# Kernel optimization log

Hardware: AMD Instinct MI355X
Metric: run time of the kernel (lower is better)

Reference implementation:

```python
import jax, jax.numpy as jnp
import numpy as np

EMBED_DIM = 1024
NUM_HEADS = 16
HEAD_DIM = EMBED_DIM // NUM_HEADS
ROPE_BASE = 10000.0


def _rope_cos_sin(seq_len, dim, dtype=jnp.float32):
    inv_freq = 1.0 / (ROPE_BASE ** (jnp.arange(0, dim, 2, dtype=jnp.float32) / dim))
    pos = jnp.arange(seq_len, dtype=jnp.float32)
    freqs = jnp.outer(pos, inv_freq)              # [S, dim/2]
    emb = jnp.concatenate([freqs, freqs], axis=-1)  # [S, dim]
    return jnp.cos(emb).astype(dtype), jnp.sin(emb).astype(dtype)


def _rotate_half(x):
    half = x.shape[-1] // 2
    return jnp.concatenate([-x[..., half:], x[..., :half]], axis=-1)


def setup_inputs() -> dict:
    key = jax.random.key(0)
    ks = jax.random.split(key, 12)
    B, S, E = 4, 2048, EMBED_DIM
    std = 1.0 / np.sqrt(E)
    inp = {
        'query': jax.random.normal(ks[0], (B, S, E), jnp.float32),
        'key': jax.random.normal(ks[1], (B, S, E), jnp.float32),
        'value': jax.random.normal(ks[2], (B, S, E), jnp.float32),
        'Wq': jax.random.uniform(ks[3], (E, E), jnp.float32, -std, std),
        'bq': jax.random.uniform(ks[4], (E,), jnp.float32, -std, std),
        'Wk': jax.random.uniform(ks[5], (E, E), jnp.float32, -std, std),
        'bk': jax.random.uniform(ks[6], (E,), jnp.float32, -std, std),
        'Wv': jax.random.uniform(ks[7], (E, E), jnp.float32, -std, std),
        'bv': jax.random.uniform(ks[8], (E,), jnp.float32, -std, std),
        'Wo': jax.random.uniform(ks[9], (E, E), jnp.float32, -std, std),
        'bo': jax.random.uniform(ks[10], (E,), jnp.float32, -std, std),
    }
    return inp


def reference(query, key, value, Wq, bq, Wk, bk, Wv, bv, Wo, bo):
    B, Sq, E = query.shape
    Sk = key.shape[1]
    H, D = NUM_HEADS, HEAD_DIM
    scale = D ** -0.5

    q = query @ Wq.T + bq
    k = key @ Wk.T + bk
    v = value @ Wv.T + bv

    # [B, H, S, D]
    q = q.reshape(B, Sq, H, D).transpose(0, 2, 1, 3)
    k = k.reshape(B, Sk, H, D).transpose(0, 2, 1, 3)
    v = v.reshape(B, Sk, H, D).transpose(0, 2, 1, 3)

    cos, sin = _rope_cos_sin(Sq, D, q.dtype)  # [S, D]; module slices by seq_len_q for both
    cos = cos[None, None]  # [1,1,S,D]
    sin = sin[None, None]
    q = q * cos + _rotate_half(q) * sin
    k = k * cos + _rotate_half(k) * sin

    scores = jnp.einsum('bhqd,bhkd->bhqk', q, k) * scale
    attn = jax.nn.softmax(scores, axis=-1)  # dropout p=0.0 -> identity
    out = jnp.einsum('bhqk,bhkd->bhqd', attn, v)
    out = out.transpose(0, 2, 1, 3).reshape(B, Sq, E)
    out = out @ Wo.T + bo
    attn_avg = attn.mean(axis=1)  # [B, Sq, Sk]
    return out, attn_avg
```

## Files before the change

kernel.cpp:

```cpp
#include <hip/hip_runtime.h>
#include <math.h>

#define TB 4
#define TS 2048
#define TE 1024
#define TH 16
#define TD 64
#define TM_ (TB*TS)

#define WS_Q   0
#define WS_K   8388608
#define WS_L   16777216
#define WS_TAB 16908288

typedef __attribute__((ext_vector_type(8))) short bf16x8;
typedef __attribute__((ext_vector_type(4))) float f32x4;

static __device__ inline unsigned fbits(float x) {
    union { float f; unsigned u; } v; v.f = x; return v.u;
}
static __device__ inline float bits2f(unsigned u) {
    union { unsigned u; float f; } v; v.u = u; return v.f;
}
static __device__ inline unsigned pack_rhu(float a, float b) {
    return __builtin_amdgcn_perm(fbits(b) + 0x8000u, fbits(a) + 0x8000u, 0x07060302u);
}
static __device__ inline short bf16s(float x) {
    return (short)((fbits(x) + 0x8000u) >> 16);
}
static __device__ inline void split2(float x0, float x1, unsigned& hp, unsigned& lp) {
    unsigned u0 = fbits(x0) + 0x8000u, u1 = fbits(x1) + 0x8000u;
    hp = __builtin_amdgcn_perm(u1, u0, 0x07060302u);
    float h0 = bits2f(u0 & 0xffff0000u);
    float h1 = bits2f(u1 & 0xffff0000u);
    lp = pack_rhu(x0 - h0, x1 - h1);
}

__global__ __launch_bounds__(256, 4)
void wsplit(const float* __restrict__ W0, const float* __restrict__ W1,
            const float* __restrict__ W2, const float* __restrict__ W3,
            short* __restrict__ dst)
{
    const int idx = blockIdx.x * 256 + threadIdx.x;
    const int t = idx & 31;
    const int n = (idx >> 5) & 1023;
    const int w = idx >> 15;
    const float* W = (w == 0) ? W0 : (w == 1) ? W1 : (w == 2) ? W2 : W3;
    const float* sp = W + (size_t)n * 1024 + t * 32;
    short* dp = dst + ((size_t)(w * 1024 + n)) * 2048 + t * 64;
    #pragma unroll
    for (int c = 0; c < 4; ++c) {
        float4 a = *(const float4*)(sp + c * 8);
        float4 b = *(const float4*)(sp + c * 8 + 4);
        unsigned H[4], L[4];
        split2(a.x, a.y, H[0], L[0]);
        split2(a.z, a.w, H[1], L[1]);
        split2(b.x, b.y, H[2], L[2]);
        split2(b.z, b.w, H[3], L[3]);
        *(uint4*)(dp + c * 8)      = make_uint4(H[0], H[1], H[2], H[3]);
        *(uint4*)(dp + 32 + c * 8) = make_uint4(L[0], L[1], L[2], L[3]);
    }
}

template<int MODE>
__global__ __launch_bounds__(256, 2)
void gemm_nt(const float* __restrict__ X, const short* __restrict__ Wsp,
             const float* __restrict__ bias, float* __restrict__ out)
{
    __shared__ short Ah[128][40], Al[128][40];
    __shared__ short Bh[128][40], Bl[128][40];

    const int tid  = threadIdx.x;
    const int lane = tid & 63;
    const int wv   = tid >> 6;
    const int t16  = lane & 15;
    const int quad = lane >> 4;
    const int wm   = (wv >> 1) * 64;
    const int wn   = (wv & 1) * 64;
    const int m0 = blockIdx.y * 128;
    const int n0 = blockIdx.x * 128;
    const int K = TE, N = TE;

    const int srow = tid >> 1;
    const int skc  = (tid & 1) * 16;
    const float* Xp = X + (size_t)(m0 + srow) * K + skc;
    const short* Wp = Wsp + (size_t)(n0 + srow) * 2048 + skc;

    f32x4 acc[4][4];
    #pragma unroll
    for (int i = 0; i < 4; ++i)
        #pragma unroll
        for (int j = 0; j < 4; ++j) acc[i][j] = (f32x4){0.f, 0.f, 0.f, 0.f};

    for (int kt = 0; kt < K; kt += 32) {
        __syncthreads();
        {
            const float* xp = Xp + kt;
            float4 x0 = *(const float4*)(xp);
            float4 x1 = *(const float4*)(xp + 4);
            float4 x2 = *(const float4*)(xp + 8);
            float4 x3 = *(const float4*)(xp + 12);
            const short* wp = Wp + kt * 2;
            uint4 wh0 = *(const uint4*)(wp);
            uint4 wh1 = *(const uint4*)(wp + 8);
            uint4 wl0 = *(const uint4*)(wp + 32);
            uint4 wl1 = *(const uint4*)(wp + 40);

            unsigned H[8], L[8];
            split2(x0.x, x0.y, H[0], L[0]);
            split2(x0.z, x0.w, H[1], L[1]);
            split2(x1.x, x1.y, H[2], L[2]);
            split2(x1.z, x1.w, H[3], L[3]);
            split2(x2.x, x2.y, H[4], L[4]);
            split2(x2.z, x2.w, H[5], L[5]);
            split2(x3.x, x3.y, H[6], L[6]);
            split2(x3.z, x3.w, H[7], L[7]);
            *(uint4*)&Ah[srow][skc]     = make_uint4(H[0], H[1], H[2], H[3]);
            *(uint4*)&Ah[srow][skc + 8] = make_uint4(H[4], H[5], H[6], H[7]);
            *(uint4*)&Al[srow][skc]     = make_uint4(L[0], L[1], L[2], L[3]);
            *(uint4*)&Al[srow][skc + 8] = make_uint4(L[4], L[5], L[6], L[7]);

            *(uint4*)&Bh[srow][skc]     = wh0;
            *(uint4*)&Bh[srow][skc + 8] = wh1;
            *(uint4*)&Bl[srow][skc]     = wl0;
            *(uint4*)&Bl[srow][skc + 8] = wl1;
        }
        __syncthreads();

        bf16x8 ah[4], al[4], bh[4], bl[4];
        #pragma unroll
        for (int i = 0; i < 4; ++i) {
            ah[i] = *(const bf16x8*)&Ah[wm + i * 16 + t16][quad * 8];
            al[i] = *(const bf16x8*)&Al[wm + i * 16 + t16][quad * 8];
            bh[i] = *(const bf16x8*)&Bh[wn + i * 16 + t16][quad * 8];
            bl[i] = *(const bf16x8*)&Bl[wn + i * 16 + t16][quad * 8];
        }
        #pragma unroll
        for (int i = 0; i < 4; ++i)
            #pragma unroll
            for (int j = 0; j < 4; ++j) {
                acc[i][j] = __builtin_amdgcn_mfma_f32_16x16x32_bf16(ah[i], bh[j], acc[i][j], 0, 0, 0);
                acc[i][j] = __builtin_amdgcn_mfma_f32_16x16x32_bf16(al[i], bh[j], acc[i][j], 0, 0, 0);
                acc[i][j] = __builtin_amdgcn_mfma_f32_16x16x32_bf16(ah[i], bl[j], acc[i][j], 0, 0, 0);
            }
    }

    if (MODE == 2) {
        short* o16 = (short*)out;
        const int b = m0 >> 11;
        const int sbase0 = (m0 & 2047) + wm + quad * 4;
        #pragma unroll
        for (int j = 0; j < 4; ++j) {
            const int n = n0 + wn + j * 16 + t16;
            const int h = n >> 6, d = n & 63;
            const float bv = bias[n];
            const size_t base = ((size_t)(b * TH + h) * TD + d) * TS;
            #pragma unroll
            for (int i = 0; i < 4; ++i) {
                const int s = sbase0 + i * 16;
                uint2 p = make_uint2(pack_rhu(acc[i][j][0] + bv, acc[i][j][1] + bv),
                                     pack_rhu(acc[i][j][2] + bv, acc[i][j][3] + bv));
                *(uint2*)(o16 + base + s) = p;
            }
        }
        return;
    }

    #pragma unroll
    for (int j = 0; j < 4; ++j) {
        const int n = n0 + wn + j * 16 + t16;
        const float bv = bias[n];
        if (MODE == 0) {
            #pragma unroll
            for (int i = 0; i < 4; ++i)
                #pragma unroll
                for (int r = 0; r < 4; ++r) {
                    const int m = m0 + wm + i * 16 + quad * 4 + r;
                    out[(size_t)m * N + n] = acc[i][j][r] + bv;
                }
        } else {
            const int h = n >> 6, d = n & 63;
            #pragma unroll
            for (int i = 0; i < 4; ++i)
                #pragma unroll
                for (int r = 0; r < 4; ++r) {
                    const int m = m0 + wm + i * 16 + quad * 4 + r;
                    const int bb_ = m >> 11, s = m & 2047;
                    out[((size_t)(bb_ * TH + h) * TS + s) * TD + d] = acc[i][j][r] + bv;
                }
        }
    }
}

__global__ void rope_table(float* __restrict__ tab)
{
    const int idx = blockIdx.x * 256 + threadIdx.x;
    const int d = idx & 31, s = idx >> 5;
    const float e = (float)(2 * d) / 64.0f;
    const float inv = 1.0f / powf(10000.0f, e);
    const float a = (float)s * inv;
    tab[2 * idx + 0] = cosf(a);
    tab[2 * idx + 1] = sinf(a);
}

__global__ __launch_bounds__(256, 2)
void rope_split(float* __restrict__ Q, float* __restrict__ Kv,
                const float* __restrict__ tab)
{
    const int idx = blockIdx.x * 256 + threadIdx.x;
    const int s  = idx & 2047;
    const int bh = (idx >> 11) & 63;
    const int qk = idx >> 17;
    float* P = qk ? Kv : Q;
    const float scale = qk ? 1.0f : (0.125f * 1.44269504f);
    const int key = qk ? (s & 7) : 0;
    unsigned* rp = (unsigned*)(P + ((size_t)bh * TS + s) * 64);

    unsigned xu[64];
    #pragma unroll
    for (int i = 0; i < 16; ++i) {
        uint4 v = *(const uint4*)(rp + i * 4);
        xu[4 * i + 0] = v.x; xu[4 * i + 1] = v.y;
        xu[4 * i + 2] = v.z; xu[4 * i + 3] = v.w;
    }
    const float* tb = tab + (size_t)s * 64;
    #pragma unroll
    for (int d = 0; d < 32; ++d) {
        const float c = tb[2 * d], sn = tb[2 * d + 1];
        const float x0 = bits2f(xu[d]), x1 = bits2f(xu[d + 32]);
        xu[d]      = fbits((x0 * c - x1 * sn) * scale);
        xu[d + 32] = fbits((x1 * c + x0 * sn) * scale);
    }
    #pragma unroll
    for (int ch = 0; ch < 8; ++ch) {
        unsigned h[4], l[4];
        #pragma unroll
        for (int p = 0; p < 4; ++p)
            split2(bits2f(xu[ch * 8 + 2 * p]), bits2f(xu[ch * 8 + 2 * p + 1]), h[p], l[p]);
        const int slot = ch ^ key;
        *(uint4*)(rp + slot * 4)      = make_uint4(h[0], h[1], h[2], h[3]);
        *(uint4*)(rp + 32 + slot * 4) = make_uint4(l[0], l[1], l[2], l[3]);
    }
}

__global__ __launch_bounds__(512, 4)
void attn_flash(const short* __restrict__ Qs, const short* __restrict__ Ks,
                const short* __restrict__ VT, float* __restrict__ O,
                float* __restrict__ Ls)
{
    __shared__ short KhL[4096], KlL[4096];
    __shared__ short VtL[4096];
    __shared__ short PsL[8192];

    const int tid  = threadIdx.x;
    const int lane = tid & 63;
    const int wv   = tid >> 6;
    const int t16  = lane & 15;
    const int quad = lane >> 4;
    const int q0w  = wv * 16;

    const int L   = blockIdx.x + 16 * blockIdx.y + 256 * blockIdx.z;
    const int xcd = L & 7;
    const int i_  = L >> 3;
    const int qt  = i_ & 15;
    const int g   = (xcd << 3) | (i_ >> 4);
    const int h   = g & 15;
    const int b   = g >> 4;

    const int q0 = qt * 128;
    const int bh = b * TH + h;
    const short* Krb = Ks + (size_t)bh * TS * 128;
    const short* Vth = VT + (size_t)bh * TD * TS;

    const int cx0 = ((quad) ^ (t16 & 7)) * 8;
    const int cx1 = ((4 + quad) ^ (t16 & 7)) * 8;

    bf16x8 qfh[2], qfl[2];
    {
        const short* qrow = Qs + ((size_t)bh * TS + q0 + q0w + t16) * 128;
        qfh[0] = *(const bf16x8*)(qrow + quad * 8);
        qfh[1] = *(const bf16x8*)(qrow + 32 + quad * 8);
        qfl[0] = *(const bf16x8*)(qrow + 64 + quad * 8);
        qfl[1] = *(const bf16x8*)(qrow + 96 + quad * 8);
    }

    float lsum[4] = {0.f, 0.f, 0.f, 0.f};
    f32x4 o_acc[4];
    #pragma unroll
    for (int dt = 0; dt < 4; ++dt) o_acc[dt] = (f32x4){0.f, 0.f, 0.f, 0.f};

    const int krow = tid >> 3;
    const int kch  = tid & 7;
    const int ksl  = (kch ^ (krow & 7)) * 8;

    uint4 rkh = *(const uint4*)(Krb + (size_t)krow * 128 + kch * 8);
    uint4 rkl = *(const uint4*)(Krb + (size_t)krow * 128 + 64 + kch * 8);
    uint4 rvv = *(const uint4*)(Vth + (size_t)krow * TS + kch * 8);

    for (int j0 = 0; j0 < TS; j0 += 64) {
        __syncthreads();
        *(uint4*)&KhL[krow * 64 + kch * 8] = rkh;
        *(uint4*)&KlL[krow * 64 + kch * 8] = rkl;
        *(uint4*)&VtL[krow * 64 + ksl]     = rvv;
        __syncthreads();

        if (j0 + 64 < TS) {
            const short* kr = Krb + (size_t)(j0 + 64 + krow) * 128;
            rkh = *(const uint4*)(kr + kch * 8);
            rkl = *(const uint4*)(kr + 64 + kch * 8);
            rvv = *(const uint4*)(Vth + (size_t)krow * TS + j0 + 64 + kch * 8);
        }

        f32x4 sc[4];
        #pragma unroll
        for (int t = 0; t < 4; ++t) sc[t] = (f32x4){0.f, 0.f, 0.f, 0.f};
        #pragma unroll
        for (int t = 0; t < 4; ++t) {
            const int rb = (t * 16 + t16) * 64;
            bf16x8 kh0 = *(const bf16x8*)&KhL[rb + cx0];
            bf16x8 kl0 = *(const bf16x8*)&KlL[rb + cx0];
            sc[t] = __builtin_amdgcn_mfma_f32_16x16x32_bf16(qfh[0], kh0, sc[t], 0, 0, 0);
            sc[t] = __builtin_amdgcn_mfma_f32_16x16x32_bf16(qfh[0], kl0, sc[t], 0, 0, 0);
            sc[t] = __builtin_amdgcn_mfma_f32_16x16x32_bf16(qfl[0], kh0, sc[t], 0, 0, 0);
            bf16x8 kh1 = *(const bf16x8*)&KhL[rb + cx1];
            bf16x8 kl1 = *(const bf16x8*)&KlL[rb + cx1];
            sc[t] = __builtin_amdgcn_mfma_f32_16x16x32_bf16(qfh[1], kh1, sc[t], 0, 0, 0);
            sc[t] = __builtin_amdgcn_mfma_f32_16x16x32_bf16(qfh[1], kl1, sc[t], 0, 0, 0);
            sc[t] = __builtin_amdgcn_mfma_f32_16x16x32_bf16(qfl[1], kh1, sc[t], 0, 0, 0);
        }

        #pragma unroll
        for (int t = 0; t < 4; ++t) {
            float p0 = __builtin_amdgcn_exp2f(sc[t][0]);
            float p1 = __builtin_amdgcn_exp2f(sc[t][1]);
            float p2 = __builtin_amdgcn_exp2f(sc[t][2]);
            float p3 = __builtin_amdgcn_exp2f(sc[t][3]);
            lsum[0] += p0; lsum[1] += p1; lsum[2] += p2; lsum[3] += p3;
            const int cb = 2 * t + (t16 >> 3);
            const int co = t16 & 7;
            const int r0 = q0w + quad * 4;
            PsL[(r0 + 0) * 64 + ((cb ^ ((r0 + 0) & 7)) * 8) + co] = bf16s(p0);
            PsL[(r0 + 1) * 64 + ((cb ^ ((r0 + 1) & 7)) * 8) + co] = bf16s(p1);
            PsL[(r0 + 2) * 64 + ((cb ^ ((r0 + 2) & 7)) * 8) + co] = bf16s(p2);
            PsL[(r0 + 3) * 64 + ((cb ^ ((r0 + 3) & 7)) * 8) + co] = bf16s(p3);
        }

        {
            const int pr = (q0w + t16) * 64;
            bf16x8 pa0 = *(const bf16x8*)&PsL[pr + cx0];
            #pragma unroll
            for (int dt = 0; dt < 4; ++dt) {
                bf16x8 vb = *(const bf16x8*)&VtL[(dt * 16 + t16) * 64 + cx0];
                o_acc[dt] = __builtin_amdgcn_mfma_f32_16x16x32_bf16(pa0, vb, o_acc[dt], 0, 0, 0);
            }
            bf16x8 pa1 = *(const bf16x8*)&PsL[pr + cx1];
            #pragma unroll
            for (int dt = 0; dt < 4; ++dt) {
                bf16x8 vb = *(const bf16x8*)&VtL[(dt * 16 + t16) * 64 + cx1];
                o_acc[dt] = __builtin_amdgcn_mfma_f32_16x16x32_bf16(pa1, vb, o_acc[dt], 0, 0, 0);
            }
        }
    }

    #pragma unroll
    for (int r = 0; r < 4; ++r) {
        #pragma unroll
        for (int off = 1; off < 16; off <<= 1)
            lsum[r] += __shfl_xor(lsum[r], off, 16);
    }

    #pragma unroll
    for (int r = 0; r < 4; ++r) {
        const int row = q0 + q0w + quad * 4 + r;
        const float inv = 1.0f / lsum[r];
        #pragma unroll
        for (int dt = 0; dt < 4; ++dt)
            O[((size_t)(b * TS) + row) * TE + h * TD + dt * 16 + t16] = o_acc[dt][r] * inv;
        if (t16 == 0)
            Ls[(size_t)bh * TS + row] = lsum[r];
    }
}

__global__ __launch_bounds__(256, 2)
void attn_avg_k(const short* __restrict__ Qs, const short* __restrict__ Ks,
                const float* __restrict__ Ls, float* __restrict__ AV)
{
    __shared__ short Qt[128][72];
    __shared__ short Kt[128][72];
    __shared__ float ML[TH][128];

    const int tid  = threadIdx.x;
    const int lane = tid & 63;
    const int wv   = tid >> 6;
    const int t16  = lane & 15;
    const int quad = lane >> 4;
    const int wq = (wv >> 1) * 64;
    const int wj = (wv & 1) * 64;

    const int j0 = blockIdx.x * 128;
    const int q0 = blockIdx.y * 128;
    const int b  = blockIdx.z;

    #pragma unroll
    for (int i = 0; i < 8; ++i) {
        const int u = tid + 256 * i;
        const int h = u >> 7, r = u & 127;
        ML[h][r] = 1.0f / Ls[(size_t)(b * TH + h) * TS + q0 + r];
    }

    f32x4 acc[4][4];
    #pragma unroll
    for (int mt = 0; mt < 4; ++mt)
        #pragma unroll
        for (int nt = 0; nt < 4; ++nt) acc[mt][nt] = (f32x4){0.f, 0.f, 0.f, 0.f};

    for (int h = 0; h < TH; ++h) {
        __syncthreads();
        const size_t rbq = (size_t)(b * TH + h) * TS + q0;
        const size_t rbk = (size_t)(b * TH + h) * TS + j0;
        #pragma unroll
        for (int i = 0; i < 4; ++i) {
            const int f = tid + 256 * i;
            const int row = f >> 3, c = f & 7;
            *(uint4*)&Qt[row][c * 8] =
                *(const uint4*)(Qs + (rbq + row) * 128 + c * 8);
            *(uint4*)&Kt[row][(c ^ (row & 7)) * 8] =
                *(const uint4*)(Ks + (rbk + row) * 128 + c * 8);
        }
        __syncthreads();

        f32x4 sc[4][4];
        #pragma unroll
        for (int mt = 0; mt < 4; ++mt)
            #pragma unroll
            for (int nt = 0; nt < 4; ++nt) sc[mt][nt] = (f32x4){0.f, 0.f, 0.f, 0.f};
        #pragma unroll
        for (int ks = 0; ks < 2; ++ks) {
            bf16x8 af[4], bf[4];
            #pragma unroll
            for (int mt = 0; mt < 4; ++mt)
                af[mt] = *(const bf16x8*)&Qt[wq + mt * 16 + t16][ks * 32 + quad * 8];
            #pragma unroll
            for (int nt = 0; nt < 4; ++nt)
                bf[nt] = *(const bf16x8*)&Kt[wj + nt * 16 + t16][ks * 32 + quad * 8];
            #pragma unroll
            for (int mt = 0; mt < 4; ++mt)
                #pragma unroll
                for (int nt = 0; nt < 4; ++nt)
                    sc[mt][nt] = __builtin_amdgcn_mfma_f32_16x16x32_bf16(af[mt], bf[nt], sc[mt][nt], 0, 0, 0);
        }

        #pragma unroll
        for (int mt = 0; mt < 4; ++mt) {
            const int rl = wq + mt * 16 + quad * 4;
            const float lv[4] = {ML[h][rl], ML[h][rl + 1], ML[h][rl + 2], ML[h][rl + 3]};
            #pragma unroll
            for (int nt = 0; nt < 4; ++nt)
                #pragma unroll
                for (int r = 0; r < 4; ++r)
                    acc[mt][nt][r] = fmaf(__builtin_amdgcn_exp2f(sc[mt][nt][r]), lv[r], acc[mt][nt][r]);
        }
    }

    const float inv_h = 1.0f / (float)TH;
    #pragma unroll
    for (int mt = 0; mt < 4; ++mt) {
        #pragma unroll
        for (int r = 0; r < 4; ++r) {
            const int row = q0 + wq + mt * 16 + quad * 4 + r;
            #pragma unroll
            for (int nt = 0; nt < 4; ++nt) {
                const int col = j0 + wj + nt * 16 + t16;
                AV[((size_t)b * TS + row) * TS + col] = acc[mt][nt][r] * inv_h;
            }
        }
    }
}

extern "C" void kernel_launch(void* const* d_in, const int* in_sizes, int n_in,
                              void* d_out, int out_size, void* d_ws, size_t ws_size,
                              hipStream_t stream)
{
    const float* query = (const float*)d_in[0];
    const float* key   = (const float*)d_in[1];
    const float* value = (const float*)d_in[2];
    const float* Wq = (const float*)d_in[3];
    const float* bq = (const float*)d_in[4];
    const float* Wk = (const float*)d_in[5];
    const float* bk = (const float*)d_in[6];
    const float* Wv = (const float*)d_in[7];
    const float* bv = (const float*)d_in[8];
    const float* Wo = (const float*)d_in[9];
    const float* bo = (const float*)d_in[10];

    float* ws  = (float*)d_ws;
    float* Qr  = ws + WS_Q;
    float* Kr  = ws + WS_K;
    float* Lsf = ws + WS_L;
    float* tab = ws + WS_TAB;

    float* out  = (float*)d_out;
    float* attn = out + (size_t)TB * TS * TE;
    short* VT   = (short*)attn;
    float* Ow   = attn + 4194304;
    short* Wsp4 = (short*)(attn + 12582912);

    dim3 blk(256);
    dim3 gproj(TE / 128, TM_ / 128);

    wsplit<<<dim3(512), blk, 0, stream>>>(Wq, Wk, Wv, Wo, Wsp4);
    rope_table<<<dim3(256), blk, 0, stream>>>(tab);

    gemm_nt<1><<<gproj, blk, 0, stream>>>(query, Wsp4,               bq, Qr);
    gemm_nt<1><<<gproj, blk, 0, stream>>>(key,   Wsp4 + 2097152,     bk, Kr);
    gemm_nt<2><<<gproj, blk, 0, stream>>>(value, Wsp4 + 2 * 2097152, bv, (float*)VT);

    rope_split<<<dim3(1024), blk, 0, stream>>>(Qr, Kr, tab);

    attn_flash<<<dim3(TS / 128, TH, TB), dim3(512), 0, stream>>>(
        (const short*)Qr, (const short*)Kr, VT, Ow, Lsf);

    gemm_nt<0><<<gproj, blk, 0, stream>>>(Ow, Wsp4 + 3 * 2097152, bo, out);

    attn_avg_k<<<dim3(TS / 128, TS / 128, TB), blk, 0, stream>>>(
        (const short*)Qr, (const short*)Kr, Lsf, attn);
}
```

Before: 685.7 us.

## Pre-split activations to bf16 hi/lo and stream tiles via direct global-to-LDS loads

Adds an xsplit kernel that converts each GEMM input into interleaved bf16 hi/lo tiles with an XOR swizzle before each projection. gemm_nt and attn_avg_k then fill LDS with global_load_lds 16-byte transfers into unpadded swizzled tiles, removing the per-iteration float loads, split arithmetic and register-staged LDS stores. The GEMM occupancy hint rises from 2 to 3, and attn_avg_k remaps block IDs so each XCD handles one batch and half of the query rows. The cost is extra launches and an extra read/write pass over each activation, with one split done in place on the Ow buffer. The Q layout in rope_split is also swizzled to match.

```diff
diff --git a/kernel.cpp b/kernel.cpp
--- a/kernel.cpp
+++ b/kernel.cpp
@@ -36,39 +36,72 @@
     lp = pack_rhu(x0 - h0, x1 - h1);
 }
 
+static __device__ inline void gl_lds16(const short* g, short* lds_base, int lane)
+{
+#if __has_builtin(__builtin_amdgcn_global_load_lds)
+    __builtin_amdgcn_global_load_lds(
+        (const __attribute__((address_space(1))) unsigned int*)g,
+        (__attribute__((address_space(3))) unsigned int*)lds_base, 16, 0, 0);
+#else
+    *(uint4*)(lds_base + lane * 8) = *(const uint4*)g;
+#endif
+}
+
+static __device__ inline void split_tile(const float* sp, short* dp, int key)
+{
+    unsigned H[16], L[16];
+    #pragma unroll
+    for (int c2 = 0; c2 < 8; ++c2) {
+        float4 v = *(const float4*)(sp + c2 * 4);
+        split2(v.x, v.y, H[2 * c2],     L[2 * c2]);
+        split2(v.z, v.w, H[2 * c2 + 1], L[2 * c2 + 1]);
+    }
+    #pragma unroll
+    for (int c = 0; c < 4; ++c) {
+        *(uint4*)(dp + ((c ^ key) * 8)) =
+            make_uint4(H[4 * c], H[4 * c + 1], H[4 * c + 2], H[4 * c + 3]);
+        *(uint4*)(dp + (((4 + c) ^ key) * 8)) =
+            make_uint4(L[4 * c], L[4 * c + 1], L[4 * c + 2], L[4 * c + 3]);
+    }
+}
+
+__global__ __launch_bounds__(256, 4)
+void xsplit(const float* src, short* dst)
+{
+    const int idx = blockIdx.x * 256 + threadIdx.x;
+    const int kt = idx & 15;
+    const int row = idx >> 4;
+    const float* sp = src + (size_t)row * 1024 + kt * 64;
+    short* dp = dst + (size_t)row * 2048 + kt * 128;
+    const int key = row & 7;
+    split_tile(sp,      dp,      key);
+    split_tile(sp + 32, dp + 64, key);
+}
+
 __global__ __launch_bounds__(256, 4)
 void wsplit(const float* __restrict__ W0, const float* __restrict__ W1,
             const float* __restrict__ W2, const float* __restrict__ W3,
             short* __restrict__ dst)
 {
     const int idx = blockIdx.x * 256 + threadIdx.x;
-    const int t = idx & 31;
-    const int n = (idx >> 5) & 1023;
-    const int w = idx >> 15;
-    const float* W = (w == 0) ? W0 : (w == 1) ? W1 : (w == 2) ? W2 : W3;
-    const float* sp = W + (size_t)n * 1024 + t * 32;
-    short* dp = dst + ((size_t)(w * 1024 + n)) * 2048 + t * 64;
-    #pragma unroll
-    for (int c = 0; c < 4; ++c) {
-        float4 a = *(const float4*)(sp + c * 8);
-        float4 b = *(const float4*)(sp + c * 8 + 4);
-        unsigned H[4], L[4];
-        split2(a.x, a.y, H[0], L[0]);
-        split2(a.z, a.w, H[1], L[1]);
-        split2(b.x, b.y, H[2], L[2]);
-        split2(b.z, b.w, H[3], L[3]);
-        *(uint4*)(dp + c * 8)      = make_uint4(H[0], H[1], H[2], H[3]);
-        *(uint4*)(dp + 32 + c * 8) = make_uint4(L[0], L[1], L[2], L[3]);
-    }
+    const int kt = idx & 15;
+    const int row = idx >> 4;
+    const int w = row >> 10, n = row & 1023;
+    const float* Wx = (w == 0) ? W0 : (w == 1) ? W1 : (w == 2) ? W2 : W3;
+    const float* sp = Wx + (size_t)n * 1024 + kt * 64;
+    short* dp = dst + (size_t)row * 2048 + kt * 128;
+    const int key = n & 7;
+    split_tile(sp,      dp,      key);
+    split_tile(sp + 32, dp + 64, key);
 }
 
 template<int MODE>
-__global__ __launch_bounds__(256, 2)
-void gemm_nt(const float* __restrict__ X, const short* __restrict__ Wsp,
+__global__ __launch_bounds__(256, 3)
+void gemm_nt(const short* __restrict__ Xs, const short* __restrict__ Ws,
              const float* __restrict__ bias, float* __restrict__ out)
 {
-    __shared__ short Ah[128][40], Al[128][40];
-    __shared__ short Bh[128][40], Bl[128][40];
+    __shared__ short A2[128 * 64];
+    __shared__ short B2[128 * 64];
 
     const int tid  = threadIdx.x;
     const int lane = tid & 63;
@@ -79,12 +112,11 @@
     const int wn   = (wv & 1) * 64;
     const int m0 = blockIdx.y * 128;
     const int n0 = blockIdx.x * 128;
-    const int K = TE, N = TE;
-
-    const int srow = tid >> 1;
-    const int skc  = (tid & 1) * 16;
-    const float* Xp = X + (size_t)(m0 + srow) * K + skc;
-    const short* Wp = Wsp + (size_t)(n0 + srow) * 2048 + skc;
+
+    const int grow = wv * 8 + (lane >> 3);
+    const int gso  = (lane & 7) * 8;
+    const int cxh = ((quad) ^ (t16 & 7)) * 8;
+    const int cxl = ((4 + quad) ^ (t16 & 7)) * 8;
 
     f32x4 acc[4][4];
     #pragma unroll
@@ -92,48 +124,24 @@
         #pragma unroll
         for (int j = 0; j < 4; ++j) acc[i][j] = (f32x4){0.f, 0.f, 0.f, 0.f};
 
-    for (int kt = 0; kt < K; kt += 32) {
+    for (int kt = 0; kt < 32; ++kt) {
         __syncthreads();
-        {
-            const float* xp = Xp + kt;
-            float4 x0 = *(const float4*)(xp);
-            float4 x1 = *(const float4*)(xp + 4);
-            float4 x2 = *(const float4*)(xp + 8);
-            float4 x3 = *(const float4*)(xp + 12);
-            const short* wp = Wp + kt * 2;
-            uint4 wh0 = *(const uint4*)(wp);
-            uint4 wh1 = *(const uint4*)(wp + 8);
-            uint4 wl0 = *(const uint4*)(wp + 32);
-            uint4 wl1 = *(const uint4*)(wp + 40);
-
-            unsigned H[8], L[8];
-            split2(x0.x, x0.y, H[0], L[0]);
-            split2(x0.z, x0.w, H[1], L[1]);
-            split2(x1.x, x1.y, H[2], L[2]);
-            split2(x1.z, x1.w, H[3], L[3]);
-            split2(x2.x, x2.y, H[4], L[4]);
-            split2(x2.z, x2.w, H[5], L[5]);
-            split2(x3.x, x3.y, H[6], L[6]);
-            split2(x3.z, x3.w, H[7], L[7]);
-            *(uint4*)&Ah[srow][skc]     = make_uint4(H[0], H[1], H[2], H[3]);
-            *(uint4*)&Ah[srow][skc + 8] = make_uint4(H[4], H[5], H[6], H[7]);
-            *(uint4*)&Al[srow][skc]     = make_uint4(L[0], L[1], L[2], L[3]);
-            *(uint4*)&Al[srow][skc + 8] = make_uint4(L[4], L[5], L[6], L[7]);
-
-            *(uint4*)&Bh[srow][skc]     = wh0;
-            *(uint4*)&Bh[srow][skc + 8] = wh1;
-            *(uint4*)&Bl[srow][skc]     = wl0;
-            *(uint4*)&Bl[srow][skc + 8] = wl1;
+        #pragma unroll
+        for (int r = 0; r < 4; ++r) {
+            gl_lds16(Xs + (size_t)(m0 + r * 32 + grow) * 2048 + kt * 64 + gso,
+                     &A2[(r * 32 + wv * 8) * 64], lane);
+            gl_lds16(Ws + (size_t)(n0 + r * 32 + grow) * 2048 + kt * 64 + gso,
+                     &B2[(r * 32 + wv * 8) * 64], lane);
         }
         __syncthreads();
 
         bf16x8 ah[4], al[4], bh[4], bl[4];
         #pragma unroll
         for (int i = 0; i < 4; ++i) {
-            ah[i] = *(const bf16x8*)&Ah[wm + i * 16 + t16][quad * 8];
-            al[i] = *(const bf16x8*)&Al[wm + i * 16 + t16][quad * 8];
-            bh[i] = *(const bf16x8*)&Bh[wn + i * 16 + t16][quad * 8];
-            bl[i] = *(const bf16x8*)&Bl[wn + i * 16 + t16][quad * 8];
+            ah[i] = *(const bf16x8*)&A2[(wm + i * 16 + t16) * 64 + cxh];
+            al[i] = *(const bf16x8*)&A2[(wm + i * 16 + t16) * 64 + cxl];
+            bh[i] = *(const bf16x8*)&B2[(wn + i * 16 + t16) * 64 + cxh];
+            bl[i] = *(const bf16x8*)&B2[(wn + i * 16 + t16) * 64 + cxl];
         }
         #pragma unroll
         for (int i = 0; i < 4; ++i)
@@ -176,7 +184,7 @@
                 #pragma unroll
                 for (int r = 0; r < 4; ++r) {
                     const int m = m0 + wm + i * 16 + quad * 4 + r;
-                    out[(size_t)m * N + n] = acc[i][j][r] + bv;
+                    out[(size_t)m * TE + n] = acc[i][j][r] + bv;
                 }
         } else {
             const int h = n >> 6, d = n & 63;
@@ -213,7 +221,7 @@
     const int qk = idx >> 17;
     float* P = qk ? Kv : Q;
     const float scale = qk ? 1.0f : (0.125f * 1.44269504f);
-    const int key = qk ? (s & 7) : 0;
+    const int key = s & 7;
     unsigned* rp = (unsigned*)(P + ((size_t)bh * TS + s) * 64);
 
     unsigned xu[64];
@@ -278,10 +286,10 @@
     bf16x8 qfh[2], qfl[2];
     {
         const short* qrow = Qs + ((size_t)bh * TS + q0 + q0w + t16) * 128;
-        qfh[0] = *(const bf16x8*)(qrow + quad * 8);
-        qfh[1] = *(const bf16x8*)(qrow + 32 + quad * 8);
-        qfl[0] = *(const bf16x8*)(qrow + 64 + quad * 8);
-        qfl[1] = *(const bf16x8*)(qrow + 96 + quad * 8);
+        qfh[0] = *(const bf16x8*)(qrow + cx0);
+        qfh[1] = *(const bf16x8*)(qrow + cx1);
+        qfl[0] = *(const bf16x8*)(qrow + 64 + cx0);
+        qfl[1] = *(const bf16x8*)(qrow + 64 + cx1);
     }
 
     float lsum[4] = {0.f, 0.f, 0.f, 0.f};
@@ -385,8 +393,8 @@
 void attn_avg_k(const short* __restrict__ Qs, const short* __restrict__ Ks,
                 const float* __restrict__ Ls, float* __restrict__ AV)
 {
-    __shared__ short Qt[128][72];
-    __shared__ short Kt[128][72];
+    __shared__ short Qt[128 * 64];
+    __shared__ short Kt[128 * 64];
     __shared__ float ML[TH][128];
 
     const int tid  = threadIdx.x;
@@ -397,16 +405,24 @@
     const int wq = (wv >> 1) * 64;
     const int wj = (wv & 1) * 64;
 
-    const int j0 = blockIdx.x * 128;
-    const int q0 = blockIdx.y * 128;
-    const int b  = blockIdx.z;
+    const int id  = blockIdx.x + 16 * blockIdx.y + 256 * blockIdx.z;
+    const int xcd = id & 7;
+    const int r_  = id >> 3;
+    const int b   = xcd >> 1;
+    const int q0  = ((xcd & 1) * 8 + (r_ >> 4)) * 128;
+    const int j0  = (r_ & 15) * 128;
 
     #pragma unroll
     for (int i = 0; i < 8; ++i) {
         const int u = tid + 256 * i;
-        const int h = u >> 7, r = u & 127;
-        ML[h][r] = 1.0f / Ls[(size_t)(b * TH + h) * TS + q0 + r];
-    }
+        const int h = u >> 7, rr = u & 127;
+        ML[h][rr] = 1.0f / Ls[(size_t)(b * TH + h) * TS + q0 + rr];
+    }
+
+    const int grow = wv * 8 + (lane >> 3);
+    const int gso  = (lane & 7) * 8;
+    const int cxh = ((quad) ^ (t16 & 7)) * 8;
+    const int cxl = ((4 + quad) ^ (t16 & 7)) * 8;
 
     f32x4 acc[4][4];
     #pragma unroll
@@ -419,13 +435,11 @@
         const size_t rbq = (size_t)(b * TH + h) * TS + q0;
         const size_t rbk = (size_t)(b * TH + h) * TS + j0;
         #pragma unroll
-        for (int i = 0; i < 4; ++i) {
-            const int f = tid + 256 * i;
-            const int row = f >> 3, c = f & 7;
-            *(uint4*)&Qt[row][c * 8] =
-                *(const uint4*)(Qs + (rbq + row) * 128 + c * 8);
-            *(uint4*)&Kt[row][(c ^ (row & 7)) * 8] =
-                *(const uint4*)(Ks + (rbk + row) * 128 + c * 8);
+        for (int r = 0; r < 4; ++r) {
+            gl_lds16(Qs + (rbq + r * 32 + grow) * 128 + gso,
+                     &Qt[(r * 32 + wv * 8) * 64], lane);
+            gl_lds16(Ks + (rbk + r * 32 + grow) * 128 + gso,
+                     &Kt[(r * 32 + wv * 8) * 64], lane);
         }
         __syncthreads();
 
@@ -436,13 +450,14 @@
             for (int nt = 0; nt < 4; ++nt) sc[mt][nt] = (f32x4){0.f, 0.f, 0.f, 0.f};
         #pragma unroll
         for (int ks = 0; ks < 2; ++ks) {
+            const int cx = ks ? cxl : cxh;
             bf16x8 af[4], bf[4];
             #pragma unroll
             for (int mt = 0; mt < 4; ++mt)
-                af[mt] = *(const bf16x8*)&Qt[wq + mt * 16 + t16][ks * 32 + quad * 8];
+                af[mt] = *(const bf16x8*)&Qt[(wq + mt * 16 + t16) * 64 + cx];
             #pragma unroll
             for (int nt = 0; nt < 4; ++nt)
-                bf[nt] = *(const bf16x8*)&Kt[wj + nt * 16 + t16][ks * 32 + quad * 8];
+                bf[nt] = *(const bf16x8*)&Kt[(wj + nt * 16 + t16) * 64 + cx];
             #pragma unroll
             for (int mt = 0; mt < 4; ++mt)
                 #pragma unroll
@@ -503,24 +518,29 @@
     float* attn = out + (size_t)TB * TS * TE;
     short* VT   = (short*)attn;
     float* Ow   = attn + 4194304;
+    short* Xsp  = (short*)Ow;
     short* Wsp4 = (short*)(attn + 12582912);
 
     dim3 blk(256);
     dim3 gproj(TE / 128, TM_ / 128);
 
-    wsplit<<<dim3(512), blk, 0, stream>>>(Wq, Wk, Wv, Wo, Wsp4);
+    wsplit<<<dim3(256), blk, 0, stream>>>(Wq, Wk, Wv, Wo, Wsp4);
     rope_table<<<dim3(256), blk, 0, stream>>>(tab);
 
-    gemm_nt<1><<<gproj, blk, 0, stream>>>(query, Wsp4,               bq, Qr);
-    gemm_nt<1><<<gproj, blk, 0, stream>>>(key,   Wsp4 + 2097152,     bk, Kr);
-    gemm_nt<2><<<gproj, blk, 0, stream>>>(value, Wsp4 + 2 * 2097152, bv, (float*)VT);
+    xsplit<<<dim3(512), blk, 0, stream>>>(query, Xsp);
+    gemm_nt<1><<<gproj, blk, 0, stream>>>(Xsp, Wsp4,               bq, Qr);
+    xsplit<<<dim3(512), blk, 0, stream>>>(key, Xsp);
+    gemm_nt<1><<<gproj, blk, 0, stream>>>(Xsp, Wsp4 + 2097152,     bk, Kr);
+    xsplit<<<dim3(512), blk, 0, stream>>>(value, Xsp);
+    gemm_nt<2><<<gproj, blk, 0, stream>>>(Xsp, Wsp4 + 2 * 2097152, bv, (float*)VT);
 
     rope_split<<<dim3(1024), blk, 0, stream>>>(Qr, Kr, tab);
 
     attn_flash<<<dim3(TS / 128, TH, TB), dim3(512), 0, stream>>>(
         (const short*)Qr, (const short*)Kr, VT, Ow, Lsf);
 
-    gemm_nt<0><<<gproj, blk, 0, stream>>>(Ow, Wsp4 + 3 * 2097152, bo, out);
+    xsplit<<<dim3(512), blk, 0, stream>>>(Ow, (short*)Ow);
+    gemm_nt<0><<<gproj, blk, 0, stream>>>((const short*)Ow, Wsp4 + 3 * 2097152, bo, out);
 
     attn_avg_k<<<dim3(TS / 128, TS / 128, TB), blk, 0, stream>>>(
         (const short*)Qr, (const short*)Kr, Lsf, attn);
```

Result: slower. 722.8 us (+5.4%).
